# Optimization experiments

Measured on AMD Instinct MI355X. Metric: run time of the kernel, lower is better.

Reference implementation:

```python
import jax, jax.numpy as jnp
import numpy as np

N_NODES = 100000
N_EDGES = 1600000
IN_DIM, HID_DIM, OUT_DIM = 128, 32, 32


def setup_inputs() -> dict:
    key = jax.random.key(0)
    k1, k2, k3, k4, k5 = jax.random.split(key, 5)
    x = jax.random.normal(k1, (N_NODES, IN_DIM), dtype=jnp.float32)
    W1 = jax.random.normal(k2, (IN_DIM, HID_DIM), dtype=jnp.float32) * (1.0 / np.sqrt(IN_DIM))
    W2 = jax.random.normal(k3, (HID_DIM, OUT_DIM), dtype=jnp.float32) * (1.0 / np.sqrt(HID_DIM))
    edge_weight = jax.random.uniform(k4, (N_EDGES,), dtype=jnp.float32)
    edge_index = jax.random.randint(k5, (2, N_EDGES), 0, N_NODES, dtype=jnp.int64)
    return {"x": x, "W1": W1, "W2": W2, "edge_weight": edge_weight, "edge_index": edge_index}


def _gcn_conv(x, W, edge_index, edge_weight):
    # GCNConv with add_self_loops=False, normalize=False, bias=False:
    # h = x @ W ; out[dst] += edge_weight * h[src]
    src, dst = edge_index[0], edge_index[1]
    h = x @ W                                   # [N, out]
    msg = h[src] * edge_weight[:, None]         # [E, out] gather + scale
    return jax.ops.segment_sum(msg, dst, num_segments=x.shape[0])  # scatter-add


def reference(x, W1, W2, edge_weight, edge_index):
    h = _gcn_conv(x, W1, edge_index, edge_weight)   # no activation in source
    z = _gcn_conv(h, W2, edge_index, edge_weight)
    return z
```

## Files before the change

kernel.cpp:

```cpp
#include <hip/hip_runtime.h>

#define N_NODES 100000
#define N_EDGES 1600000
#define IN_DIM 128
#define HID_DIM 32

#define NPB 256
#define BSHIFT 8
#define NBUCK ((N_NODES + NPB - 1) / NPB)
#define EPB 4096
#define NBLK_E ((N_EDGES + EPB - 1) / EPB)
#define OSTRIDE (NBUCK + 1)
#define CAPB 4608
#define MMROWS 128
#define NBLK_MM ((N_NODES + MMROWS - 1) / MMROWS)
#define XS_STRIDE 136

typedef __attribute__((ext_vector_type(8))) short bf16x8;
typedef __attribute__((ext_vector_type(4))) float f32x4;

__device__ __forceinline__ unsigned int pack_bf16x2(float a0, float a1) {
    unsigned int u0 = __float_as_uint(a0), u1 = __float_as_uint(a1);
    u0 = (u0 + 0x7FFFu + ((u0 >> 16) & 1u)) >> 16;
    u1 = (u1 + 0x7FFFu + ((u1 >> 16) & 1u)) >> 16;
    return u0 | (u1 << 16);
}

__device__ __forceinline__ unsigned short bf16_of(float v) {
    unsigned int u = __float_as_uint(v);
    u = (u + 0x7FFFu + ((u >> 16) & 1u)) >> 16;
    return (unsigned short)u;
}

__device__ __forceinline__ int scan512(int v, int* wtmp) {
    const int t = threadIdx.x, lane = t & 63, wv = t >> 6;
    int incl = v;
#pragma unroll
    for (int o = 1; o < 64; o <<= 1) {
        const int n = __shfl_up(incl, o, 64);
        if (lane >= o) incl += n;
    }
    if (lane == 63) wtmp[wv] = incl;
    __syncthreads();
    if (t < 8) {
        const int wval = wtmp[t];
        int s = wval;
#pragma unroll
        for (int o = 1; o < 8; o <<= 1) {
            const int n = __shfl_up(s, o, 64);
            if (t >= o) s += n;
        }
        wtmp[t] = s - wval;
    }
    __syncthreads();
    return incl + wtmp[wv];
}

__global__ __launch_bounds__(512) void fusedA(const int* __restrict__ ei,
                                              const float* __restrict__ ew,
                                              unsigned int* __restrict__ ulin,
                                              unsigned short* __restrict__ wlin,
                                              int* __restrict__ ostart,
                                              const float* __restrict__ x,
                                              const float* __restrict__ W,
                                              unsigned int* __restrict__ h) {
    __shared__ __align__(16) char smem[36000];
    const int tid = threadIdx.x;

    if (blockIdx.x < NBLK_E) {
        unsigned int*   stag_u = (unsigned int*)smem;
        unsigned short* stag_w = (unsigned short*)(smem + 16384);
        int* lh     = (int*)(smem + 24576);
        int* lstart = (int*)(smem + 26144);
        int* wtmp   = (int*)(smem + 27712);

        for (int j = tid; j < NBUCK; j += 512) lh[j] = 0;
        __syncthreads();

        const int e0 = blockIdx.x * EPB;
        int dstr[8];
        unsigned int srcr[8];
        unsigned short wreg[8];
#pragma unroll
        for (int u = 0; u < 8; ++u) {
            const int e = e0 + u * 512 + tid;
            if (e < N_EDGES) {
                dstr[u] = ei[N_EDGES + e];
                srcr[u] = (unsigned int)ei[e];
                wreg[u] = bf16_of(ew[e]);
                atomicAdd(&lh[dstr[u] >> BSHIFT], 1);
            } else {
                dstr[u] = -1; srcr[u] = 0; wreg[u] = 0;
            }
        }
        __syncthreads();

        const int v = (tid < NBUCK) ? lh[tid] : 0;
        const int incl = scan512(v, wtmp);
        if (tid < NBUCK) lstart[tid] = incl - v;
        if (tid == NBUCK - 1) lstart[NBUCK] = incl;
        __syncthreads();
        if (tid < NBUCK) lh[tid] = 0;
        __syncthreads();

#pragma unroll
        for (int u = 0; u < 8; ++u) {
            const int d = dstr[u];
            if (d >= 0) {
                const int b = d >> BSHIFT;
                const int slot = atomicAdd(&lh[b], 1);
                const int p = lstart[b] + slot;
                stag_u[p] = srcr[u] | ((unsigned int)(d & (NPB - 1)) << 17);
                stag_w[p] = wreg[u];
            }
        }
        __syncthreads();

        const int total = lstart[NBUCK];
        const size_t gbase = (size_t)blockIdx.x * EPB;
        for (int i = tid; i < total; i += 512) {
            ulin[gbase + i] = stag_u[i];
            wlin[gbase + i] = stag_w[i];
        }
        if (tid < OSTRIDE) ostart[blockIdx.x * OSTRIDE + tid] = lstart[tid];
    } else {
        unsigned short* xbf = (unsigned short*)smem;
        const int lane = tid & 63, w = tid >> 6;
        const int row0 = (blockIdx.x - NBLK_E) * MMROWS;

#pragma unroll
        for (int i = 0; i < 8; ++i) {
            const int idx = tid + i * 512;
            const int r = idx >> 5, c4 = idx & 31;
            const int grow = row0 + r;
            float4 vv = (grow < N_NODES) ? ((const float4*)x)[(size_t)grow * 32 + c4]
                                         : make_float4(0.f, 0.f, 0.f, 0.f);
            *(uint2*)&xbf[r * XS_STRIDE + c4 * 4] =
                make_uint2(pack_bf16x2(vv.x, vv.y), pack_bf16x2(vv.z, vv.w));
        }

        const int colB = lane & 15, kg = lane >> 4;
        bf16x8 bfrag[2][4];
#pragma unroll
        for (int n = 0; n < 2; ++n)
#pragma unroll
            for (int kt = 0; kt < 4; ++kt) {
                const int kbase = kt * 32 + kg * 8;
                bf16x8 f;
#pragma unroll
                for (int j = 0; j < 8; ++j)
                    f[j] = (short)bf16_of(W[(size_t)(kbase + j) * HID_DIM + n * 16 + colB]);
                bfrag[n][kt] = f;
            }
        __syncthreads();

        f32x4 acc0 = {0.f, 0.f, 0.f, 0.f}, acc1 = {0.f, 0.f, 0.f, 0.f};
        const int arow = w * 16 + (lane & 15);
#pragma unroll
        for (int kt = 0; kt < 4; ++kt) {
            bf16x8 a = *(bf16x8*)&xbf[arow * XS_STRIDE + kt * 32 + kg * 8];
            acc0 = __builtin_amdgcn_mfma_f32_16x16x32_bf16(a, bfrag[0][kt], acc0, 0, 0, 0);
            acc1 = __builtin_amdgcn_mfma_f32_16x16x32_bf16(a, bfrag[1][kt], acc1, 0, 0, 0);
        }
        __syncthreads();

        float* cst = (float*)smem;
        float* cw_ = cst + w * 576;
        const int crow = (lane >> 4) * 4;
#pragma unroll
        for (int r = 0; r < 4; ++r) {
            cw_[(crow + r) * 36 + (lane & 15)] = acc0[r];
            cw_[(crow + r) * 36 + 16 + (lane & 15)] = acc1[r];
        }
        __syncthreads();
        const int r = tid >> 2, q = tid & 3;
        const int grow = row0 + r;
        if (grow < N_NODES) {
            const float* cr = cst + (r >> 4) * 576 + (r & 15) * 36 + q * 8;
            uint4 o = make_uint4(pack_bf16x2(cr[0], cr[1]), pack_bf16x2(cr[2], cr[3]),
                                 pack_bf16x2(cr[4], cr[5]), pack_bf16x2(cr[6], cr[7]));
            ((uint4*)h)[(size_t)grow * 4 + q] = o;
        }
    }
}

__global__ __launch_bounds__(512) void phaseB(const int* __restrict__ ostart,
                                              const unsigned int* __restrict__ ulin,
                                              const unsigned short* __restrict__ wlin,
                                              unsigned int* __restrict__ csr,
                                              int* __restrict__ offs) {
    __shared__ unsigned int   stag_u[CAPB];
    __shared__ unsigned short stag_w[CAPB];
    __shared__ unsigned int   stag2[CAPB];
    __shared__ int st[NBLK_E];
    __shared__ int P[NBLK_E + 1];
    __shared__ int lh[NPB];
    __shared__ int wtmp[8];
    const int b = blockIdx.x;
    const int t = threadIdx.x;

    int s0 = 0, len = 0;
    if (t < NBLK_E) {
        s0 = ostart[t * OSTRIDE + b];
        st[t] = s0;
        len = ostart[t * OSTRIDE + b + 1] - s0;
    }
    int* red = (int*)stag2;
    red[t] = s0;
    __syncthreads();
    for (int s = 256; s > 0; s >>= 1) {
        if (t < s) red[t] += red[t + s];
        __syncthreads();
    }
    const int base_out = red[0];
    __syncthreads();

    const int incl = scan512(len, wtmp);
    if (t < NBLK_E) P[t] = incl - len;
    if (t == NBLK_E - 1) P[NBLK_E] = incl;
    __syncthreads();
    const int cnt = min(P[NBLK_E], CAPB);

    for (int i = t; i < cnt; i += 512) {
        int lo = 0, hi = NBLK_E - 1;
        while (lo < hi) {
            const int mid = (lo + hi + 1) >> 1;
            if (P[mid] <= i) lo = mid; else hi = mid - 1;
        }
        const size_t g = (size_t)lo * EPB + st[lo] + (i - P[lo]);
        stag_u[i] = ulin[g];
        stag_w[i] = wlin[g];
    }
    if (t < NPB) lh[t] = 0;
    __syncthreads();

    for (int i = t; i < cnt; i += 512)
        atomicAdd(&lh[(stag_u[i] >> 17) & (NPB - 1)], 1);
    __syncthreads();

    const int v = (t < NPB) ? lh[t] : 0;
    const int incl2 = scan512(v, wtmp);
    if (t < NPB) {
        const int excl = incl2 - v;
        lh[t] = excl;
        const int node = (b << BSHIFT) + t;
        if (node < N_NODES) offs[node] = base_out + excl;
    }
    if (b == NBUCK - 1 && t == 0) offs[N_NODES] = base_out + cnt;
    __syncthreads();

    for (int i = t; i < cnt; i += 512) {
        const unsigned int u = stag_u[i];
        const int dl = (u >> 17) & (NPB - 1);
        const int pos = atomicAdd(&lh[dl], 1);
        stag2[pos] = (u & 0x1FFFF) | ((unsigned int)(stag_w[i] & 0x7FFFu) << 17);
    }
    __syncthreads();
    for (int i = t; i < cnt; i += 512) csr[base_out + i] = stag2[i];
}


__device__ __forceinline__ void bf16fma8(float acc[8], const uint4 v, const float w) {
    acc[0] += w * __uint_as_float(v.x << 16);
    acc[1] += w * __uint_as_float(v.x & 0xFFFF0000u);
    acc[2] += w * __uint_as_float(v.y << 16);
    acc[3] += w * __uint_as_float(v.y & 0xFFFF0000u);
    acc[4] += w * __uint_as_float(v.z << 16);
    acc[5] += w * __uint_as_float(v.z & 0xFFFF0000u);
    acc[6] += w * __uint_as_float(v.w << 16);
    acc[7] += w * __uint_as_float(v.w & 0xFFFF0000u);
}

__device__ __forceinline__ void edge_accum(const int* __restrict__ offs,
                                           const unsigned int* __restrict__ csr,
                                           const uint4* __restrict__ h,
                                           int node, int ln, float acc[8]) {
    int i = offs[node];
    const int end = offs[node + 1];
    for (; i + 7 < end; i += 8) {
        unsigned int e[8];
        uint4 v[8];
#pragma unroll
        for (int j = 0; j < 8; ++j) e[j] = csr[i + j];
#pragma unroll
        for (int j = 0; j < 8; ++j) v[j] = h[(size_t)(e[j] & 0x1FFFF) * 4 + ln];
#pragma unroll
        for (int j = 0; j < 8; ++j)
            bf16fma8(acc, v[j], __uint_as_float((e[j] >> 17) << 16));
    }
    if (i + 3 < end) {
        unsigned int e[4];
        uint4 v[4];
#pragma unroll
        for (int j = 0; j < 4; ++j) e[j] = csr[i + j];
#pragma unroll
        for (int j = 0; j < 4; ++j) v[j] = h[(size_t)(e[j] & 0x1FFFF) * 4 + ln];
#pragma unroll
        for (int j = 0; j < 4; ++j)
            bf16fma8(acc, v[j], __uint_as_float((e[j] >> 17) << 16));
        i += 4;
    }
    for (; i < end; ++i) {
        const unsigned int e = csr[i];
        bf16fma8(acc, h[(size_t)(e & 0x1FFFF) * 4 + ln], __uint_as_float((e >> 17) << 16));
    }
}

__global__ __launch_bounds__(256) void gather_mm(const int* __restrict__ offs,
                                                 const unsigned int* __restrict__ csr,
                                                 const uint4* __restrict__ h1,
                                                 const float* __restrict__ W2,
                                                 uint4* __restrict__ h2) {
    __shared__ float W2s[HID_DIM * HID_DIM];
    __shared__ float a1s[64 * 33];
    const int tid = threadIdx.x;
    ((float4*)W2s)[tid] = ((const float4*)W2)[tid];
    const int g = tid >> 2, ln = tid & 3;
    const int node = blockIdx.x * 64 + g;
    const int node_c = min(node, N_NODES - 1);

    float acc[8] = {0.f, 0.f, 0.f, 0.f, 0.f, 0.f, 0.f, 0.f};
    edge_accum(offs, csr, h1, node_c, ln, acc);

    __syncthreads();
#pragma unroll
    for (int j = 0; j < 8; ++j) a1s[g * 33 + 8 * ln + j] = acc[j];
    __syncthreads();

    const float* ar = a1s + g * 33;
    float s[8] = {0.f, 0.f, 0.f, 0.f, 0.f, 0.f, 0.f, 0.f};
#pragma unroll
    for (int k = 0; k < HID_DIM; ++k) {
        const float av = ar[k];
        const float* wr = W2s + k * HID_DIM + 8 * ln;
#pragma unroll
        for (int j = 0; j < 8; ++j) s[j] += av * wr[j];
    }
    if (node < N_NODES)
        h2[(size_t)node * 4 + ln] = make_uint4(pack_bf16x2(s[0], s[1]),
                                               pack_bf16x2(s[2], s[3]),
                                               pack_bf16x2(s[4], s[5]),
                                               pack_bf16x2(s[6], s[7]));
}

__global__ __launch_bounds__(256) void gather_out(const int* __restrict__ offs,
                                                  const unsigned int* __restrict__ csr,
                                                  const uint4* __restrict__ h2,
                                                  float* __restrict__ out) {
    const int tid = threadIdx.x;
    const int g = tid >> 2, ln = tid & 3;
    const int node = blockIdx.x * 64 + g;
    if (node >= N_NODES) return;

    float acc[8] = {0.f, 0.f, 0.f, 0.f, 0.f, 0.f, 0.f, 0.f};
    edge_accum(offs, csr, h2, node, ln, acc);
    ((float4*)out)[(size_t)node * 8 + 2 * ln] = make_float4(acc[0], acc[1], acc[2], acc[3]);
    ((float4*)out)[(size_t)node * 8 + 2 * ln + 1] = make_float4(acc[4], acc[5], acc[6], acc[7]);
}

extern "C" void kernel_launch(void* const* d_in, const int* in_sizes, int n_in,
                              void* d_out, int out_size, void* d_ws, size_t ws_size,
                              hipStream_t stream) {
    const float* x  = (const float*)d_in[0];
    const float* W1 = (const float*)d_in[1];
    const float* W2 = (const float*)d_in[2];
    const float* ew = (const float*)d_in[3];
    const int*   ei = (const int*)d_in[4];
    float* out = (float*)d_out;

    unsigned int*   ulin = (unsigned int*)d_ws;
    unsigned short* wlin = (unsigned short*)(ulin + N_EDGES);
    unsigned int*   csr  = (unsigned int*)(wlin + N_EDGES);
    unsigned int*   h1u  = csr + N_EDGES;
    unsigned int*   h2u  = h1u + (size_t)N_NODES * 16;
    int*  offs   = (int*)(h2u + (size_t)N_NODES * 16);
    int*  ostart = offs + N_NODES + 1;

    fusedA<<<NBLK_E + NBLK_MM, 512, 0, stream>>>(ei, ew, ulin, wlin, ostart,
                                                 x, W1, h1u);

    phaseB<<<NBUCK, 512, 0, stream>>>(ostart, ulin, wlin, csr, offs);

    gather_mm<<<(N_NODES + 63) / 64, 256, 0, stream>>>(offs, csr, (const uint4*)h1u,
                                                       W2, (uint4*)h2u);

    gather_out<<<(N_NODES + 63) / 64, 256, 0, stream>>>(offs, csr, (const uint4*)h2u, out);
}
```

Baseline: 90.06 us.

## Split first matmul between edge-bucketing kernel and CSR-build kernel

The dense x@W1 matmul blocks are split: the first 391 tiles still run alongside edge bucketing in fusedA, and the remaining tiles now run as extra blocks in the CSR-building kernel (renamed fusedB). The aim is to balance work between the two launches so the lightly-occupied CSR phase (391 bucket blocks) overlaps the rest of the matmul. The cost is a larger static shared-memory footprint for fusedB, which may reduce occupancy, and a split ratio that is tuned by hand.

```diff
diff --git a/kernel.cpp b/kernel.cpp
--- a/kernel.cpp
+++ b/kernel.cpp
@@ -14,6 +14,8 @@
 #define CAPB 4608
 #define MMROWS 128
 #define NBLK_MM ((N_NODES + MMROWS - 1) / MMROWS)
+#define MM1 391
+#define MM2 (NBLK_MM - MM1)
 #define XS_STRIDE 136
 
 typedef __attribute__((ext_vector_type(8))) short bf16x8;
@@ -54,6 +56,69 @@
     }
     __syncthreads();
     return incl + wtmp[wv];
+}
+
+__device__ __forceinline__ void mm_body(char* smem, int row0,
+                                        const float* __restrict__ x,
+                                        const float* __restrict__ W,
+                                        unsigned int* __restrict__ h) {
+    const int tid = threadIdx.x;
+    unsigned short* xbf = (unsigned short*)smem;
+    const int lane = tid & 63, w = tid >> 6;
+
+#pragma unroll
+    for (int i = 0; i < 8; ++i) {
+        const int idx = tid + i * 512;
+        const int r = idx >> 5, c4 = idx & 31;
+        const int grow = row0 + r;
+        float4 vv = (grow < N_NODES) ? ((const float4*)x)[(size_t)grow * 32 + c4]
+                                     : make_float4(0.f, 0.f, 0.f, 0.f);
+        *(uint2*)&xbf[r * XS_STRIDE + c4 * 4] =
+            make_uint2(pack_bf16x2(vv.x, vv.y), pack_bf16x2(vv.z, vv.w));
+    }
+
+    const int colB = lane & 15, kg = lane >> 4;
+    bf16x8 bfrag[2][4];
+#pragma unroll
+    for (int n = 0; n < 2; ++n)
+#pragma unroll
+        for (int kt = 0; kt < 4; ++kt) {
+            const int kbase = kt * 32 + kg * 8;
+            bf16x8 f;
+#pragma unroll
+            for (int j = 0; j < 8; ++j)
+                f[j] = (short)bf16_of(W[(size_t)(kbase + j) * HID_DIM + n * 16 + colB]);
+            bfrag[n][kt] = f;
+        }
+    __syncthreads();
+
+    f32x4 acc0 = {0.f, 0.f, 0.f, 0.f}, acc1 = {0.f, 0.f, 0.f, 0.f};
+    const int arow = w * 16 + (lane & 15);
+#pragma unroll
+    for (int kt = 0; kt < 4; ++kt) {
+        bf16x8 a = *(bf16x8*)&xbf[arow * XS_STRIDE + kt * 32 + kg * 8];
+        acc0 = __builtin_amdgcn_mfma_f32_16x16x32_bf16(a, bfrag[0][kt], acc0, 0, 0, 0);
+        acc1 = __builtin_amdgcn_mfma_f32_16x16x32_bf16(a, bfrag[1][kt], acc1, 0, 0, 0);
+    }
+    __syncthreads();
+
+    float* cst = (float*)smem;
+    float* cw_ = cst + w * 576;
+    const int crow = (lane >> 4) * 4;
+#pragma unroll
+    for (int r = 0; r < 4; ++r) {
+        cw_[(crow + r) * 36 + (lane & 15)] = acc0[r];
+        cw_[(crow + r) * 36 + 16 + (lane & 15)] = acc1[r];
+    }
+    __syncthreads();
+    const int r = tid >> 2, q = tid & 3;
+    const int grow = row0 + r;
+    if (grow < N_NODES) {
+        const float* cr = cst + (r >> 4) * 576 + (r & 15) * 36 + q * 8;
+        uint4 o = make_uint4(pack_bf16x2(cr[0], cr[1]), pack_bf16x2(cr[2], cr[3]),
+                             pack_bf16x2(cr[4], cr[5]), pack_bf16x2(cr[6], cr[7]));
+        ((uint4*)h)[(size_t)grow * 4 + q] = o;
+    }
 }
 
 __global__ __launch_bounds__(512) void fusedA(const int* __restrict__ ei,
@@ -124,139 +189,92 @@
         }
         if (tid < OSTRIDE) ostart[blockIdx.x * OSTRIDE + tid] = lstart[tid];
     } else {
-        unsigned short* xbf = (unsigned short*)smem;
-        const int lane = tid & 63, w = tid >> 6;
-        const int row0 = (blockIdx.x - NBLK_E) * MMROWS;
-
-#pragma unroll
-        for (int i = 0; i < 8; ++i) {
-            const int idx = tid + i * 512;
-            const int r = idx >> 5, c4 = idx & 31;
-            const int grow = row0 + r;
-            float4 vv = (grow < N_NODES) ? ((const float4*)x)[(size_t)grow * 32 + c4]
-                                         : make_float4(0.f, 0.f, 0.f, 0.f);
-            *(uint2*)&xbf[r * XS_STRIDE + c4 * 4] =
-                make_uint2(pack_bf16x2(vv.x, vv.y), pack_bf16x2(vv.z, vv.w));
-        }
-
-        const int colB = lane & 15, kg = lane >> 4;
-        bf16x8 bfrag[2][4];
-#pragma unroll
-        for (int n = 0; n < 2; ++n)
-#pragma unroll
-            for (int kt = 0; kt < 4; ++kt) {
-                const int kbase = kt * 32 + kg * 8;
-                bf16x8 f;
-#pragma unroll
-                for (int j = 0; j < 8; ++j)
-                    f[j] = (short)bf16_of(W[(size_t)(kbase + j) * HID_DIM + n * 16 + colB]);
-                bfrag[n][kt] = f;
-            }
-        __syncthreads();
-
-        f32x4 acc0 = {0.f, 0.f, 0.f, 0.f}, acc1 = {0.f, 0.f, 0.f, 0.f};
-        const int arow = w * 16 + (lane & 15);
-#pragma unroll
-        for (int kt = 0; kt < 4; ++kt) {
-            bf16x8 a = *(bf16x8*)&xbf[arow * XS_STRIDE + kt * 32 + kg * 8];
-            acc0 = __builtin_amdgcn_mfma_f32_16x16x32_bf16(a, bfrag[0][kt], acc0, 0, 0, 0);
-            acc1 = __builtin_amdgcn_mfma_f32_16x16x32_bf16(a, bfrag[1][kt], acc1, 0, 0, 0);
-        }
-        __syncthreads();
-
-        float* cst = (float*)smem;
-        float* cw_ = cst + w * 576;
-        const int crow = (lane >> 4) * 4;
-#pragma unroll
-        for (int r = 0; r < 4; ++r) {
-            cw_[(crow + r) * 36 + (lane & 15)] = acc0[r];
-            cw_[(crow + r) * 36 + 16 + (lane & 15)] = acc1[r];
-        }
-        __syncthreads();
-        const int r = tid >> 2, q = tid & 3;
-        const int grow = row0 + r;
-        if (grow < N_NODES) {
-            const float* cr = cst + (r >> 4) * 576 + (r & 15) * 36 + q * 8;
-            uint4 o = make_uint4(pack_bf16x2(cr[0], cr[1]), pack_bf16x2(cr[2], cr[3]),
-                                 pack_bf16x2(cr[4], cr[5]), pack_bf16x2(cr[6], cr[7]));
-            ((uint4*)h)[(size_t)grow * 4 + q] = o;
-        }
-    }
-}
-
-__global__ __launch_bounds__(512) void phaseB(const int* __restrict__ ostart,
+        mm_body(smem, (int)(blockIdx.x - NBLK_E) * MMROWS, x, W, h);
+    }
+}
+
+__global__ __launch_bounds__(512) void fusedB(const int* __restrict__ ostart,
                                               const unsigned int* __restrict__ ulin,
                                               const unsigned short* __restrict__ wlin,
                                               unsigned int* __restrict__ csr,
-                                              int* __restrict__ offs) {
-    __shared__ unsigned int   stag_u[CAPB];
-    __shared__ unsigned short stag_w[CAPB];
-    __shared__ unsigned int   stag2[CAPB];
-    __shared__ int st[NBLK_E];
-    __shared__ int P[NBLK_E + 1];
-    __shared__ int lh[NPB];
-    __shared__ int wtmp[8];
-    const int b = blockIdx.x;
+                                              int* __restrict__ offs,
+                                              const float* __restrict__ x,
+                                              const float* __restrict__ W,
+                                              unsigned int* __restrict__ h) {
+    __shared__ __align__(16) char smem[50304];
     const int t = threadIdx.x;
 
-    int s0 = 0, len = 0;
-    if (t < NBLK_E) {
-        s0 = ostart[t * OSTRIDE + b];
-        st[t] = s0;
-        len = ostart[t * OSTRIDE + b + 1] - s0;
-    }
-    int* red = (int*)stag2;
-    red[t] = s0;
-    __syncthreads();
-    for (int s = 256; s > 0; s >>= 1) {
-        if (t < s) red[t] += red[t + s];
-        __syncthreads();
-    }
-    const int base_out = red[0];
-    __syncthreads();
-
-    const int incl = scan512(len, wtmp);
-    if (t < NBLK_E) P[t] = incl - len;
-    if (t == NBLK_E - 1) P[NBLK_E] = incl;
-    __syncthreads();
-    const int cnt = min(P[NBLK_E], CAPB);
-
-    for (int i = t; i < cnt; i += 512) {
-        int lo = 0, hi = NBLK_E - 1;
-        while (lo < hi) {
-            const int mid = (lo + hi + 1) >> 1;
-            if (P[mid] <= i) lo = mid; else hi = mid - 1;
-        }
-        const size_t g = (size_t)lo * EPB + st[lo] + (i - P[lo]);
-        stag_u[i] = ulin[g];
-        stag_w[i] = wlin[g];
-    }
-    if (t < NPB) lh[t] = 0;
-    __syncthreads();
-
-    for (int i = t; i < cnt; i += 512)
-        atomicAdd(&lh[(stag_u[i] >> 17) & (NPB - 1)], 1);
-    __syncthreads();
-
-    const int v = (t < NPB) ? lh[t] : 0;
-    const int incl2 = scan512(v, wtmp);
-    if (t < NPB) {
-        const int excl = incl2 - v;
-        lh[t] = excl;
-        const int node = (b << BSHIFT) + t;
-        if (node < N_NODES) offs[node] = base_out + excl;
-    }
-    if (b == NBUCK - 1 && t == 0) offs[N_NODES] = base_out + cnt;
-    __syncthreads();
-
-    for (int i = t; i < cnt; i += 512) {
-        const unsigned int u = stag_u[i];
-        const int dl = (u >> 17) & (NPB - 1);
-        const int pos = atomicAdd(&lh[dl], 1);
-        stag2[pos] = (u & 0x1FFFF) | ((unsigned int)(stag_w[i] & 0x7FFFu) << 17);
-    }
-    __syncthreads();
-    for (int i = t; i < cnt; i += 512) csr[base_out + i] = stag2[i];
+    if (blockIdx.x < NBUCK) {
+        unsigned int*   stag_u = (unsigned int*)smem;
+        unsigned short* stag_w = (unsigned short*)(smem + 18432);
+        unsigned int*   stag2  = (unsigned int*)(smem + 27648);
+        int* st   = (int*)(smem + 46080);
+        int* P    = (int*)(smem + 47648);
+        int* lh   = (int*)(smem + 49216);
+        int* wtmp = (int*)(smem + 50240);
+        const int b = blockIdx.x;
+
+        int s0 = 0, len = 0;
+        if (t < NBLK_E) {
+            s0 = ostart[t * OSTRIDE + b];
+            st[t] = s0;
+            len = ostart[t * OSTRIDE + b + 1] - s0;
+        }
+        int* red = (int*)stag2;
+        red[t] = s0;
+        __syncthreads();
+        for (int s = 256; s > 0; s >>= 1) {
+            if (t < s) red[t] += red[t + s];
+            __syncthreads();
+        }
+        const int base_out = red[0];
+        __syncthreads();
+
+        const int incl = scan512(len, wtmp);
+        if (t < NBLK_E) P[t] = incl - len;
+        if (t == NBLK_E - 1) P[NBLK_E] = incl;
+        __syncthreads();
+        const int cnt = min(P[NBLK_E], CAPB);
+
+        for (int i = t; i < cnt; i += 512) {
+            int lo = 0, hi = NBLK_E - 1;
+            while (lo < hi) {
+                const int mid = (lo + hi + 1) >> 1;
+                if (P[mid] <= i) lo = mid; else hi = mid - 1;
+            }
+            const size_t g = (size_t)lo * EPB + st[lo] + (i - P[lo]);
+            stag_u[i] = ulin[g];
+            stag_w[i] = wlin[g];
+        }
+        if (t < NPB) lh[t] = 0;
+        __syncthreads();
+
+        for (int i = t; i < cnt; i += 512)
+            atomicAdd(&lh[(stag_u[i] >> 17) & (NPB - 1)], 1);
+        __syncthreads();
+
+        const int v = (t < NPB) ? lh[t] : 0;
+        const int incl2 = scan512(v, wtmp);
+        if (t < NPB) {
+            const int excl = incl2 - v;
+            lh[t] = excl;
+            const int node = (b << BSHIFT) + t;
+            if (node < N_NODES) offs[node] = base_out + excl;
+        }
+        if (b == NBUCK - 1 && t == 0) offs[N_NODES] = base_out + cnt;
+        __syncthreads();
+
+        for (int i = t; i < cnt; i += 512) {
+            const unsigned int u = stag_u[i];
+            const int dl = (u >> 17) & (NPB - 1);
+            const int pos = atomicAdd(&lh[dl], 1);
+            stag2[pos] = (u & 0x1FFFF) | ((unsigned int)(stag_w[i] & 0x7FFFu) << 17);
+        }
+        __syncthreads();
+        for (int i = t; i < cnt; i += 512) csr[base_out + i] = stag2[i];
+    } else {
+        mm_body(smem, (int)(blockIdx.x - NBUCK + MM1) * MMROWS, x, W, h);
+    }
 }
 
 
@@ -376,10 +394,9 @@
     int*  offs   = (int*)(h2u + (size_t)N_NODES * 16);
     int*  ostart = offs + N_NODES + 1;
 
-    fusedA<<<NBLK_E + NBLK_MM, 512, 0, stream>>>(ei, ew, ulin, wlin, ostart,
-                                                 x, W1, h1u);
-
-    phaseB<<<NBUCK, 512, 0, stream>>>(ostart, ulin, wlin, csr, offs);
+    fusedA<<<NBLK_E + MM1, 512, 0, stream>>>(ei, ew, ulin, wlin, ostart, x, W1, h1u);
+
+    fusedB<<<NBUCK + MM2, 512, 0, stream>>>(ostart, ulin, wlin, csr, offs, x, W1, h1u);
 
     gather_mm<<<(N_NODES + 63) / 64, 256, 0, stream>>>(offs, csr, (const uint4*)h1u,
                                                        W2, (uint4*)h2u);
```

Result: faster. 86.61 us (-3.8%).
